# Kernel tuning notes

Measured on AMD Instinct MI355X. Metric: run time of the kernel, lower is better.

Reference implementation:

```python
import jax, jax.numpy as jnp
import numpy as np

B, L, D = 1, 4096, 1024
H = 16
HD = D // H
SCALE = HD ** -0.5


def setup_inputs() -> dict:
    key = jax.random.key(0)
    k1, k2, k3 = jax.random.split(key, 3)
    X = jax.random.normal(k1, (B, L, D), dtype=jnp.float32)
    # torch Linear default init ~ U(-1/sqrt(fan_in), 1/sqrt(fan_in)); scaled normals are fine for a reference
    Wqkv = jax.random.normal(k2, (D, 3 * D), dtype=jnp.float32) * (D ** -0.5)
    bqkv = jnp.zeros((3 * D,), dtype=jnp.float32)
    Wproj = jax.random.normal(k3, (D, D), dtype=jnp.float32) * (D ** -0.5)
    bproj = jnp.zeros((D,), dtype=jnp.float32)
    return {"X": X, "Wqkv": Wqkv, "bqkv": bqkv, "Wproj": Wproj, "bproj": bproj}


def reference(X, Wqkv, bqkv, Wproj, bproj):
    Bn, Ln, Dn = X.shape
    qkv = X @ Wqkv + bqkv                       # [B, L, 3D]
    qkv = qkv.reshape(Bn, Ln, 3, H, HD)
    q, k, v = qkv[:, :, 0], qkv[:, :, 1], qkv[:, :, 2]   # [B, L, H, HD]
    # attention scores [B, H, L, L] (naive, matches original)
    attn = jnp.einsum('bqhd,bkhd->bhqk', q, k) * SCALE
    causal = jnp.tril(jnp.ones((Ln, Ln), dtype=bool))     # True = keep
    attn = jnp.where(causal, attn, -jnp.inf)
    score = jax.nn.softmax(attn, axis=-1)
    out = jnp.einsum('bhqk,bkhd->bqhd', score, v)         # [B, L, H, HD]
    out = out.reshape(Bn, Ln, Dn)
    return out @ Wproj + bproj
```

## Files before the change

### kernel.cpp

```cpp
#include <hip/hip_runtime.h>
#include <hip/hip_bf16.h>
#include <string.h>


typedef unsigned short ushort_t;
typedef __attribute__((ext_vector_type(8))) short short8;
typedef __attribute__((ext_vector_type(4))) float f32x4;

#define MFMA16(a, b, c) __builtin_amdgcn_mfma_f32_16x16x32_bf16(a, b, c, 0, 0, 0)

static constexpr int Lq = 4096;
static constexpr int Dm = 1024;
static constexpr int NH = 16;
static constexpr int HD = 64;
static constexpr int D3 = 3072;
static constexpr float SCALE_LOG2E = 0.125f * 1.44269504088896340736f;

__device__ __forceinline__ ushort_t f2bf(float f) {
    union { float f; unsigned int u; } x{f};
    unsigned int u = x.u;
    u += 0x7fffu + ((u >> 16) & 1u);
    return (ushort_t)(u >> 16);
}

__device__ __forceinline__ unsigned int cvtpk(float a, float b) {
    __hip_bfloat162 h = __float22bfloat162_rn(make_float2(a, b));
    unsigned int u;
    memcpy(&u, &h, 4);
    return u;
}

__device__ __forceinline__ void gl2lds16(const ushort_t* g, ushort_t* l) {
    __builtin_amdgcn_global_load_lds(
        (const __attribute__((address_space(1))) unsigned int*)g,
        (__attribute__((address_space(3))) unsigned int*)l, 16, 0, 0);
}

__global__ void __launch_bounds__(256)
prep(const float* __restrict__ X, const float* __restrict__ Wqkv,
     const float* __restrict__ Wproj, ushort_t* __restrict__ Xb,
     ushort_t* __restrict__ WqkvT, ushort_t* __restrict__ WprojT) {
    __shared__ float tile[32][33];
    const int bid = blockIdx.x, tid = threadIdx.x;
    if (bid < 4096) {
        int i = (bid * 256 + tid) * 4;
        float4 v = *(const float4*)&X[i];
        ushort_t r[4] = { f2bf(v.x), f2bf(v.y), f2bf(v.z), f2bf(v.w) };
        *(uint2*)&Xb[i] = *(uint2*)r;
        return;
    }
    const float* W; ushort_t* Wt; int Nd, nb, kb;
    if (bid < 7168) {
        int b = bid - 4096; W = Wqkv;  Wt = WqkvT;  Nd = 3072;
        nb = (b % 96) * 32; kb = (b / 96) * 32;
    } else {
        int b = bid - 7168; W = Wproj; Wt = WprojT; Nd = 1024;
        nb = (b % 32) * 32; kb = (b / 32) * 32;
    }
    const int tx = tid & 31, ty = tid >> 5;
    for (int j = 0; j < 32; j += 8)
        tile[ty + j][tx] = W[(size_t)(kb + ty + j) * Nd + nb + tx];
    __syncthreads();
    for (int j = 0; j < 32; j += 8)
        Wt[(size_t)(nb + ty + j) * Dm + kb + tx] = f2bf(tile[tx][ty + j]);
}

__global__ void __launch_bounds__(256)
gemm_qkv(const ushort_t* __restrict__ A, const ushort_t* __restrict__ Bt,
         const float* __restrict__ bias, ushort_t* __restrict__ Cq,
         ushort_t* __restrict__ Vt) {
    __shared__ alignas(16) ushort_t Alds[128 * 32];
    __shared__ alignas(16) ushort_t Blds[128 * 32];
    const int tid  = threadIdx.x;
    const int lane = tid & 63;
    const int w    = tid >> 6;
    const int quad = lane >> 4;
    const int l16  = lane & 15;
    const int mbase = blockIdx.x * 128;
    const int nbase = blockIdx.y * 128;
    const int moff  = (w >> 1) * 64;
    const int noff  = (w & 1) * 64;
    const int K = Dm;

    f32x4 acc[4][4] = {};

    for (int kb = 0; kb < K; kb += 32) {
        __syncthreads();
        #pragma unroll
        for (int c = 0; c < 2; c++) {
            int id  = w * 128 + c * 64 + lane;
            int row = id >> 2, col = (id & 3) * 8;
            gl2lds16(&A[(size_t)(mbase + row) * K + kb + col], &Alds[(size_t)(w * 128 + c * 64) * 8]);
            gl2lds16(&Bt[(size_t)(nbase + row) * K + kb + col], &Blds[(size_t)(w * 128 + c * 64) * 8]);
        }
        __syncthreads();
        short8 a[4], b[4];
        #pragma unroll
        for (int m = 0; m < 4; m++)
            a[m] = *(const short8*)&Alds[(moff + m * 16 + l16) * 32 + quad * 8];
        #pragma unroll
        for (int n = 0; n < 4; n++)
            b[n] = *(const short8*)&Blds[(noff + n * 16 + l16) * 32 + quad * 8];
        #pragma unroll
        for (int m = 0; m < 4; m++)
            #pragma unroll
            for (int n = 0; n < 4; n++)
                acc[m][n] = MFMA16(a[m], b[n], acc[m][n]);
    }

    if (nbase < 2048) {
        const bool qscale = (nbase < 1024);
        #pragma unroll
        for (int m = 0; m < 4; m++)
            #pragma unroll
            for (int n = 0; n < 4; n++)
                #pragma unroll
                for (int r = 0; r < 4; r++) {
                    int row = mbase + moff + m * 16 + quad * 4 + r;
                    int col = nbase + noff + n * 16 + l16;
                    float v = acc[m][n][r] + bias[col];
                    if (qscale) v *= SCALE_LOG2E;
                    Cq[(size_t)row * D3 + col] = f2bf(v);
                }
    } else {
        const int dbase = nbase - 2048 + noff;
        const size_t kb0 = (size_t)mbase + moff;
        #pragma unroll
        for (int n = 0; n < 4; n++) {
            const float bv = bias[nbase + noff + n * 16 + l16];
            ushort_t* vrow = Vt + (size_t)(dbase + n * 16 + l16) * Lq + kb0 + quad * 16;
            #pragma unroll
            for (int rp = 0; rp < 2; rp++) {
                ushort_t pk[8];
                #pragma unroll
                for (int dr = 0; dr < 2; dr++)
                    #pragma unroll
                    for (int m = 0; m < 4; m++)
                        pk[dr * 4 + m] = f2bf(acc[m][n][2 * rp + dr] + bv);
                *(short8*)(vrow + rp * 8) = *(const short8*)pk;
            }
        }
    }
}

__global__ void __launch_bounds__(512, 2)
attn_fwd(const ushort_t* __restrict__ qkv, const ushort_t* __restrict__ Vt,
         ushort_t* __restrict__ O) {
    __shared__ alignas(16) ushort_t Kl[2][2][64 * 64];
    __shared__ alignas(16) ushort_t Vl[2][2][64 * 64];
    __shared__ alignas(16) ushort_t Pl[8 * 32 * 72];
    __shared__ alignas(16) float    Ml[256 * 41];

    const int tid  = threadIdx.x;
    const int lane = tid & 63;
    const int w    = tid >> 6;
    const int half = w >> 2;
    const int sub  = w & 3;
    const int quad = lane >> 4;
    const int l16  = lane & 15;
    const int bid  = blockIdx.x;
    const int h    = bid & 15;
    const int p    = bid >> 4;
    ushort_t* pw   = Pl + w * 32 * 72;
    const float NEG_INF = -__builtin_inff();
    const int sw   = l16 & 7;

    const short bf1 = (short)0x3F80;
    const short8 ones = { bf1, bf1, bf1, bf1, bf1, bf1, bf1, bf1 };

    const ushort_t* kbase = qkv + Dm + h * HD;
    const ushort_t* vbase = Vt + (size_t)h * HD * Lq;

    int kvo[4][2];
    #pragma unroll
    for (int s = 0; s < 4; s++)
        #pragma unroll
        for (int kh = 0; kh < 2; kh++)
            kvo[s][kh] = (s * 16 + l16) * 64 + (((kh * 4 + quad) ^ sw) * 8);

    const int rr = tid >> 3, cc = (tid & 7) ^ (rr & 7);
    const ushort_t* kse = kbase + (size_t)rr * D3 + cc * 8;
    const ushort_t* vse = vbase + (size_t)rr * Lq + cc * 8;
    const int dstoff = w * 512;

    for (int sel = 0; sel < 2; sel++) {
        const int c      = sel ? (31 - p) : p;
        const int qc     = c * 128;
        const int rounds = c + 1;
        const int qw     = qc + sub * 32;

        short8 qf[2][2];
        #pragma unroll
        for (int m = 0; m < 2; m++) {
            const ushort_t* qr = qkv + (size_t)(qw + m * 16 + l16) * D3 + h * HD;
            qf[m][0] = *(const short8*)(qr + quad * 8);
            qf[m][1] = *(const short8*)(qr + 32 + quad * 8);
        }

        f32x4 o[2][4] = {};
        f32x4 lacc[2] = {};

        const ushort_t* kp = kse;
        const ushort_t* vp = vse;

        auto stage = [&](int b) {
            gl2lds16(kp,           &Kl[0][b][dstoff]);
            gl2lds16(kp + 64 * D3, &Kl[1][b][dstoff]);
            gl2lds16(vp,           &Vl[0][b][dstoff]);
            gl2lds16(vp + 64,      &Vl[1][b][dstoff]);
            kp += (size_t)128 * D3;
            vp += 128;
        };

        stage(0);

        for (int r = 0; r < rounds; r++) {
            const int buf = r & 1;
            __syncthreads();
            if (r + 1 < rounds) stage(buf ^ 1);

            const ushort_t* Kb = &Kl[half][buf][0];
            const ushort_t* Vb = &Vl[half][buf][0];
            const int k0 = (2 * r + half) * 64;
            const bool domask = (r == rounds - 1);

            short8 kf[4][2];
            #pragma unroll
            for (int s = 0; s < 4; s++)
                #pragma unroll
                for (int kh = 0; kh < 2; kh++)
                    kf[s][kh] = *(const short8*)&Kb[kvo[s][kh]];

            f32x4 st[2][4];
            #pragma unroll
            for (int m = 0; m < 2; m++)
                #pragma unroll
                for (int s = 0; s < 4; s++) {
                    f32x4 t = {};
                    t = MFMA16(qf[m][0], kf[s][0], t);
                    t = MFMA16(qf[m][1], kf[s][1], t);
                    st[m][s] = t;
                }

            #pragma unroll
            for (int m = 0; m < 2; m++)
                #pragma unroll
                for (int r4 = 0; r4 < 4; r4++) {
                    float e[4];
                    #pragma unroll
                    for (int s = 0; s < 4; s++) {
                        float v = st[m][s][r4];
                        if (domask) {
                            const int qg = qw + m * 16 + quad * 4 + r4;
                            if (k0 + s * 16 + l16 > qg) v = NEG_INF;
                        }
                        e[s] = __builtin_amdgcn_exp2f(v);
                    }
                    uint2 pk = { cvtpk(e[0], e[1]), cvtpk(e[2], e[3]) };
                    *(uint2*)&pw[(m * 16 + quad * 4 + r4) * 72 + l16 * 4] = pk;
                }

            short8 pf[2][2];
            #pragma unroll
            for (int m = 0; m < 2; m++)
                #pragma unroll
                for (int kh = 0; kh < 2; kh++)
                    pf[m][kh] = *(const short8*)&pw[(m * 16 + l16) * 72 + kh * 32 + quad * 8];
            #pragma unroll
            for (int m = 0; m < 2; m++) {
                lacc[m] = MFMA16(pf[m][0], ones, lacc[m]);
                lacc[m] = MFMA16(pf[m][1], ones, lacc[m]);
            }

            short8 vf[4][2];
            #pragma unroll
            for (int t = 0; t < 4; t++)
                #pragma unroll
                for (int kh = 0; kh < 2; kh++)
                    vf[t][kh] = *(const short8*)&Vb[kvo[t][kh]];
            #pragma unroll
            for (int m = 0; m < 2; m++)
                #pragma unroll
                for (int t = 0; t < 4; t++) {
                    o[m][t] = MFMA16(pf[m][0], vf[t][0], o[m][t]);
                    o[m][t] = MFMA16(pf[m][1], vf[t][1], o[m][t]);
                }
        }

        __syncthreads();
        if (half == 1) {
            float* dst = Ml + (sub * 64 + lane) * 41;
            #pragma unroll
            for (int m = 0; m < 2; m++)
                #pragma unroll
                for (int t = 0; t < 4; t++)
                    *(f32x4*)(dst + m * 16 + t * 4) = o[m][t];
            *(f32x4*)(dst + 32) = lacc[0];
            *(f32x4*)(dst + 36) = lacc[1];
        }
        __syncthreads();
        if (half == 0) {
            const float* src = Ml + (sub * 64 + lane) * 41;
            #pragma unroll
            for (int m = 0; m < 2; m++)
                #pragma unroll
                for (int t = 0; t < 4; t++)
                    o[m][t] += *(const f32x4*)(src + m * 16 + t * 4);
            lacc[0] += *(const f32x4*)(src + 32);
            lacc[1] += *(const f32x4*)(src + 36);
            #pragma unroll
            for (int m = 0; m < 2; m++)
                #pragma unroll
                for (int r4 = 0; r4 < 4; r4++) {
                    const float inv = 1.0f / lacc[m][r4];
                    ushort_t* orow = O + (size_t)(qw + m * 16 + quad * 4 + r4) * Dm + h * HD;
                    #pragma unroll
                    for (int t = 0; t < 4; t++)
                        orow[t * 16 + l16] = f2bf(o[m][t][r4] * inv);
                }
        }
        __syncthreads();
    }
}

__global__ void __launch_bounds__(256)
gemm_proj(const ushort_t* __restrict__ A, const ushort_t* __restrict__ Bt,
          const float* __restrict__ bias, float* __restrict__ C) {
    __shared__ alignas(16) ushort_t Alds[128 * 32];
    __shared__ alignas(16) ushort_t Blds[64 * 32];
    const int tid  = threadIdx.x;
    const int lane = tid & 63;
    const int w    = tid >> 6;
    const int quad = lane >> 4;
    const int l16  = lane & 15;
    const int mbase = blockIdx.x * 128;
    const int nbase = blockIdx.y * 64;
    const int moff  = (w >> 1) * 64;
    const int noff  = (w & 1) * 32;
    const int K = Dm, N = Dm;

    f32x4 acc[4][2] = {};

    for (int kb = 0; kb < K; kb += 32) {
        __syncthreads();
        #pragma unroll
        for (int c = 0; c < 2; c++) {
            int id  = w * 128 + c * 64 + lane;
            int row = id >> 2, col = (id & 3) * 8;
            gl2lds16(&A[(size_t)(mbase + row) * K + kb + col], &Alds[(size_t)(w * 128 + c * 64) * 8]);
        }
        {
            int id  = w * 64 + lane;
            int row = id >> 2, col = (id & 3) * 8;
            gl2lds16(&Bt[(size_t)(nbase + row) * K + kb + col], &Blds[(size_t)(w * 64) * 8]);
        }
        __syncthreads();
        short8 a[4], b[2];
        #pragma unroll
        for (int m = 0; m < 4; m++)
            a[m] = *(const short8*)&Alds[(moff + m * 16 + l16) * 32 + quad * 8];
        #pragma unroll
        for (int n = 0; n < 2; n++)
            b[n] = *(const short8*)&Blds[(noff + n * 16 + l16) * 32 + quad * 8];
        #pragma unroll
        for (int m = 0; m < 4; m++)
            #pragma unroll
            for (int n = 0; n < 2; n++)
                acc[m][n] = MFMA16(a[m], b[n], acc[m][n]);
    }

    #pragma unroll
    for (int m = 0; m < 4; m++)
        #pragma unroll
        for (int n = 0; n < 2; n++)
            #pragma unroll
            for (int r = 0; r < 4; r++) {
                int row = mbase + moff + m * 16 + quad * 4 + r;
                int col = nbase + noff + n * 16 + l16;
                C[(size_t)row * N + col] = acc[m][n][r] + bias[col];
            }
}

extern "C" void kernel_launch(void* const* d_in, const int* in_sizes, int n_in,
                              void* d_out, int out_size, void* d_ws, size_t ws_size,
                              hipStream_t stream) {
    const float* X     = (const float*)d_in[0];
    const float* Wqkv  = (const float*)d_in[1];
    const float* bqkv  = (const float*)d_in[2];
    const float* Wproj = (const float*)d_in[3];
    const float* bproj = (const float*)d_in[4];
    float* out = (float*)d_out;

    ushort_t* ws     = (ushort_t*)d_ws;
    ushort_t* Xb     = ws;
    ushort_t* WqkvT  = Xb + (size_t)Lq * Dm;
    ushort_t* WprojT = WqkvT + (size_t)D3 * Dm;
    ushort_t* qkvB   = WprojT + (size_t)Dm * Dm;
    ushort_t* VtB    = qkvB + (size_t)Lq * D3;
    ushort_t* Ob     = VtB + (size_t)NH * HD * Lq;

    prep<<<dim3(8192), 256, 0, stream>>>(X, Wqkv, Wproj, Xb, WqkvT, WprojT);

    gemm_qkv<<<dim3(Lq / 128, D3 / 128), 256, 0, stream>>>(
        Xb, WqkvT, bqkv, qkvB, VtB);

    attn_fwd<<<dim3(256), 512, 0, stream>>>(qkvB, VtB, Ob);

    gemm_proj<<<dim3(Lq / 128, Dm / 64), 256, 0, stream>>>(
        Ob, WprojT, bproj, out);
}
```

Measured before the change: 215.2 us.

## Keep P in registers via transposed S=K·Q and 16x16x16 MFMA in attention

Computes scores transposed (K as A operand) so the softmax probabilities come out in a register layout usable directly as the B operand of a 16x16x16 bf16 MFMA for P·V, removing the per-wave P round-trip through LDS and the ones-MFMA row-sum, which is replaced by a register sum plus lane shuffles. The block grows to 1024 threads with four wave groups splitting the KV tile, K and V staging are split across thread halves, and the three-way partial reduction reuses the KV LDS through a union. It risks lower occupancy (one block per CU), halved MFMA K-depth for P·V, and relies on an inline-asm fallback with manual nops when the builtin is missing.

```diff
diff --git a/kernel.cpp b/kernel.cpp
--- a/kernel.cpp
+++ b/kernel.cpp
@@ -5,9 +5,24 @@
 
 typedef unsigned short ushort_t;
 typedef __attribute__((ext_vector_type(8))) short short8;
+typedef __attribute__((ext_vector_type(4))) short short4_t;
 typedef __attribute__((ext_vector_type(4))) float f32x4;
 
 #define MFMA16(a, b, c) __builtin_amdgcn_mfma_f32_16x16x32_bf16(a, b, c, 0, 0, 0)
+
+#if __has_builtin(__builtin_amdgcn_mfma_f32_16x16x16bf16_1k)
+#define HAVE_MFMA16K 1
+__device__ __forceinline__ f32x4 mfma16x16(short4_t a, short4_t b, f32x4 c) {
+    return __builtin_amdgcn_mfma_f32_16x16x16bf16_1k(a, b, c, 0, 0, 0);
+}
+#else
+#define HAVE_MFMA16K 0
+__device__ __forceinline__ f32x4 mfma16x16(short4_t a, short4_t b, f32x4 c) {
+    asm("s_nop 1\n\tv_mfma_f32_16x16x16_bf16 %0, %1, %2, %0"
+        : "+v"(c) : "v"(a), "v"(b));
+    return c;
+}
+#endif
 
 static constexpr int Lq = 4096;
 static constexpr int Dm = 1024;
@@ -143,71 +158,87 @@
     }
 }
 
-__global__ void __launch_bounds__(512, 2)
+__global__ void __launch_bounds__(1024)
 attn_fwd(const ushort_t* __restrict__ qkv, const ushort_t* __restrict__ Vt,
          ushort_t* __restrict__ O) {
-    __shared__ alignas(16) ushort_t Kl[2][2][64 * 64];
-    __shared__ alignas(16) ushort_t Vl[2][2][64 * 64];
-    __shared__ alignas(16) ushort_t Pl[8 * 32 * 72];
-    __shared__ alignas(16) float    Ml[256 * 41];
+    union SMem {
+        struct { ushort_t K[2][2][64 * 64]; ushort_t V[2][2][64 * 64]; } kv;
+        float Ml[3 * 256 * 35];
+    };
+    __shared__ SMem sm;
 
     const int tid  = threadIdx.x;
     const int lane = tid & 63;
     const int w    = tid >> 6;
-    const int half = w >> 2;
+    const int qtr  = w >> 2;
     const int sub  = w & 3;
     const int quad = lane >> 4;
     const int l16  = lane & 15;
     const int bid  = blockIdx.x;
     const int h    = bid & 15;
     const int p    = bid >> 4;
-    ushort_t* pw   = Pl + w * 32 * 72;
     const float NEG_INF = -__builtin_inff();
-    const int sw   = l16 & 7;
-
-    const short bf1 = (short)0x3F80;
-    const short8 ones = { bf1, bf1, bf1, bf1, bf1, bf1, bf1, bf1 };
 
     const ushort_t* kbase = qkv + Dm + h * HD;
     const ushort_t* vbase = Vt + (size_t)h * HD * Lq;
 
-    int kvo[4][2];
+    int koff[2][2];
     #pragma unroll
-    for (int s = 0; s < 4; s++)
+    for (int s = 0; s < 2; s++) {
+        const int tok = (l16 & 3) * 16 + (qtr & 1) * 8 + s * 4 + (l16 >> 2);
+        const int fk  = ((l16 & 3) << 1) | ((l16 >> 2) & 1);
         #pragma unroll
         for (int kh = 0; kh < 2; kh++)
-            kvo[s][kh] = (s * 16 + l16) * 64 + (((kh * 4 + quad) ^ sw) * 8);
-
-    const int rr = tid >> 3, cc = (tid & 7) ^ (rr & 7);
-    const ushort_t* kse = kbase + (size_t)rr * D3 + cc * 8;
-    const ushort_t* vse = vbase + (size_t)rr * Lq + cc * 8;
-    const int dstoff = w * 512;
+            koff[s][kh] = tok * 64 + (((kh * 4 + quad) ^ fk) * 8);
+    }
+    int voff[4][2];
+    #pragma unroll
+    for (int t4 = 0; t4 < 4; t4++)
+        #pragma unroll
+        for (int s = 0; s < 2; s++) {
+            const int row = t4 * 16 + l16;
+            const int g = (qtr & 1) * 4 + s * 2 + (quad >> 1);
+            voff[t4][s] = row * 64 + ((g ^ (l16 & 7)) * 8) + (quad & 1) * 4;
+        }
+    const int kmc = (qtr >> 1) * 64 + (qtr & 1) * 8 + quad;
+
+    const int  tv  = tid & 511;
+    const int  rr  = tv >> 3;
+    const int  ccK = (tv & 7) ^ ((((rr >> 4) & 3) << 1) | (rr & 1));
+    const int  ccV = (tv & 7) ^ (rr & 7);
+    const bool isK = (tid < 512);
+    const int  dsto = (w & 7) * 512;
+    const ushort_t* kse = kbase + (size_t)rr * D3 + ccK * 8;
+    const ushort_t* vse = vbase + (size_t)rr * Lq + ccV * 8;
 
     for (int sel = 0; sel < 2; sel++) {
         const int c      = sel ? (31 - p) : p;
         const int qc     = c * 128;
         const int rounds = c + 1;
-        const int qw     = qc + sub * 32;
+        const int qrow0  = qc + sub * 32;
 
         short8 qf[2][2];
         #pragma unroll
         for (int m = 0; m < 2; m++) {
-            const ushort_t* qr = qkv + (size_t)(qw + m * 16 + l16) * D3 + h * HD;
+            const ushort_t* qr = qkv + (size_t)(qrow0 + m * 16 + l16) * D3 + h * HD;
             qf[m][0] = *(const short8*)(qr + quad * 8);
             qf[m][1] = *(const short8*)(qr + 32 + quad * 8);
         }
 
         f32x4 o[2][4] = {};
-        f32x4 lacc[2] = {};
+        float sacc[2] = { 0.f, 0.f };
 
         const ushort_t* kp = kse;
         const ushort_t* vp = vse;
 
         auto stage = [&](int b) {
-            gl2lds16(kp,           &Kl[0][b][dstoff]);
-            gl2lds16(kp + 64 * D3, &Kl[1][b][dstoff]);
-            gl2lds16(vp,           &Vl[0][b][dstoff]);
-            gl2lds16(vp + 64,      &Vl[1][b][dstoff]);
+            if (isK) {
+                gl2lds16(kp,           &sm.kv.K[0][b][dsto]);
+                gl2lds16(kp + 64 * D3, &sm.kv.K[1][b][dsto]);
+            } else {
+                gl2lds16(vp,           &sm.kv.V[0][b][dsto]);
+                gl2lds16(vp + 64,      &sm.kv.V[1][b][dsto]);
+            }
             kp += (size_t)128 * D3;
             vp += 128;
         };
@@ -219,105 +250,98 @@
             __syncthreads();
             if (r + 1 < rounds) stage(buf ^ 1);
 
-            const ushort_t* Kb = &Kl[half][buf][0];
-            const ushort_t* Vb = &Vl[half][buf][0];
-            const int k0 = (2 * r + half) * 64;
+            const ushort_t* Kb = &sm.kv.K[qtr >> 1][buf][0];
+            const ushort_t* Vb = &sm.kv.V[qtr >> 1][buf][0];
             const bool domask = (r == rounds - 1);
 
-            short8 kf[4][2];
-            #pragma unroll
-            for (int s = 0; s < 4; s++)
+            short8 kf[2][2];
+            #pragma unroll
+            for (int s = 0; s < 2; s++)
                 #pragma unroll
                 for (int kh = 0; kh < 2; kh++)
-                    kf[s][kh] = *(const short8*)&Kb[kvo[s][kh]];
-
-            f32x4 st[2][4];
-            #pragma unroll
-            for (int m = 0; m < 2; m++)
-                #pragma unroll
-                for (int s = 0; s < 4; s++) {
+                    kf[s][kh] = *(const short8*)&Kb[koff[s][kh]];
+
+            short4_t pT[2][2];
+            #pragma unroll
+            for (int m = 0; m < 2; m++) {
+                const int qg = qrow0 + m * 16 + l16;
+                #pragma unroll
+                for (int s = 0; s < 2; s++) {
                     f32x4 t = {};
-                    t = MFMA16(qf[m][0], kf[s][0], t);
-                    t = MFMA16(qf[m][1], kf[s][1], t);
-                    st[m][s] = t;
-                }
-
-            #pragma unroll
-            for (int m = 0; m < 2; m++)
-                #pragma unroll
-                for (int r4 = 0; r4 < 4; r4++) {
+                    t = MFMA16(kf[s][0], qf[m][0], t);
+                    t = MFMA16(kf[s][1], qf[m][1], t);
                     float e[4];
                     #pragma unroll
-                    for (int s = 0; s < 4; s++) {
-                        float v = st[m][s][r4];
-                        if (domask) {
-                            const int qg = qw + m * 16 + quad * 4 + r4;
-                            if (k0 + s * 16 + l16 > qg) v = NEG_INF;
-                        }
-                        e[s] = __builtin_amdgcn_exp2f(v);
+                    for (int r4 = 0; r4 < 4; r4++) {
+                        float v = t[r4];
+                        if (domask && (r * 128 + kmc + s * 4 + r4 * 16 > qg))
+                            v = NEG_INF;
+                        e[r4] = __builtin_amdgcn_exp2f(v);
                     }
-                    uint2 pk = { cvtpk(e[0], e[1]), cvtpk(e[2], e[3]) };
-                    *(uint2*)&pw[(m * 16 + quad * 4 + r4) * 72 + l16 * 4] = pk;
+                    sacc[m] += (e[0] + e[1]) + (e[2] + e[3]);
+                    union { unsigned int u[2]; short4_t s4; } pb;
+                    pb.u[0] = cvtpk(e[0], e[1]);
+                    pb.u[1] = cvtpk(e[2], e[3]);
+                    pT[m][s] = pb.s4;
                 }
-
-            short8 pf[2][2];
+            }
+
+            #pragma unroll
+            for (int t4 = 0; t4 < 4; t4++)
+                #pragma unroll
+                for (int s = 0; s < 2; s++) {
+                    short4_t vf = *(const short4_t*)&Vb[voff[t4][s]];
+                    o[0][t4] = mfma16x16(vf, pT[0][s], o[0][t4]);
+                    o[1][t4] = mfma16x16(vf, pT[1][s], o[1][t4]);
+                }
+        }
+
+#if !HAVE_MFMA16K
+        asm volatile("s_nop 7\n\ts_nop 7" ::: "memory");
+#endif
+        #pragma unroll
+        for (int m = 0; m < 2; m++) {
+            sacc[m] += __shfl_xor(sacc[m], 16);
+            sacc[m] += __shfl_xor(sacc[m], 32);
+        }
+
+        __syncthreads();
+        if (qtr != 0) {
+            float* dst = sm.Ml + (size_t)((qtr - 1) * 256 + sub * 64 + lane) * 35;
             #pragma unroll
             for (int m = 0; m < 2; m++)
                 #pragma unroll
-                for (int kh = 0; kh < 2; kh++)
-                    pf[m][kh] = *(const short8*)&pw[(m * 16 + l16) * 72 + kh * 32 + quad * 8];
+                for (int t4 = 0; t4 < 4; t4++)
+                    *(f32x4*)(dst + (m * 4 + t4) * 4) = o[m][t4];
+            dst[32] = sacc[0];
+            dst[33] = sacc[1];
+        }
+        __syncthreads();
+        if (qtr == 0) {
+            #pragma unroll
+            for (int j = 0; j < 3; j++) {
+                const float* src = sm.Ml + (size_t)(j * 256 + sub * 64 + lane) * 35;
+                #pragma unroll
+                for (int m = 0; m < 2; m++)
+                    #pragma unroll
+                    for (int t4 = 0; t4 < 4; t4++)
+                        o[m][t4] += *(const f32x4*)(src + (m * 4 + t4) * 4);
+                sacc[0] += src[32];
+                sacc[1] += src[33];
+            }
             #pragma unroll
             for (int m = 0; m < 2; m++) {
-                lacc[m] = MFMA16(pf[m][0], ones, lacc[m]);
-                lacc[m] = MFMA16(pf[m][1], ones, lacc[m]);
-            }
-
-            short8 vf[4][2];
-            #pragma unroll
-            for (int t = 0; t < 4; t++)
-                #pragma unroll
-                for (int kh = 0; kh < 2; kh++)
-                    vf[t][kh] = *(const short8*)&Vb[kvo[t][kh]];
-            #pragma unroll
-            for (int m = 0; m < 2; m++)
-                #pragma unroll
-                for (int t = 0; t < 4; t++) {
-                    o[m][t] = MFMA16(pf[m][0], vf[t][0], o[m][t]);
-                    o[m][t] = MFMA16(pf[m][1], vf[t][1], o[m][t]);
+                const float inv = 1.0f / sacc[m];
+                ushort_t* orow = O + (size_t)(qrow0 + m * 16 + l16) * Dm + h * HD;
+                #pragma unroll
+                for (int t4 = 0; t4 < 4; t4++) {
+                    ushort_t pk[4];
+                    #pragma unroll
+                    for (int r4 = 0; r4 < 4; r4++)
+                        pk[r4] = f2bf(o[m][t4][r4] * inv);
+                    *(uint2*)(orow + t4 * 16 + quad * 4) = *(const uint2*)pk;
                 }
-        }
-
-        __syncthreads();
-        if (half == 1) {
-            float* dst = Ml + (sub * 64 + lane) * 41;
-            #pragma unroll
-            for (int m = 0; m < 2; m++)
-                #pragma unroll
-                for (int t = 0; t < 4; t++)
-                    *(f32x4*)(dst + m * 16 + t * 4) = o[m][t];
-            *(f32x4*)(dst + 32) = lacc[0];
-            *(f32x4*)(dst + 36) = lacc[1];
-        }
-        __syncthreads();
-        if (half == 0) {
-            const float* src = Ml + (sub * 64 + lane) * 41;
-            #pragma unroll
-            for (int m = 0; m < 2; m++)
-                #pragma unroll
-                for (int t = 0; t < 4; t++)
-                    o[m][t] += *(const f32x4*)(src + m * 16 + t * 4);
-            lacc[0] += *(const f32x4*)(src + 32);
-            lacc[1] += *(const f32x4*)(src + 36);
-            #pragma unroll
-            for (int m = 0; m < 2; m++)
-                #pragma unroll
-                for (int r4 = 0; r4 < 4; r4++) {
-                    const float inv = 1.0f / lacc[m][r4];
-                    ushort_t* orow = O + (size_t)(qw + m * 16 + quad * 4 + r4) * Dm + h * HD;
-                    #pragma unroll
-                    for (int t = 0; t < 4; t++)
-                        orow[t * 16 + l16] = f2bf(o[m][t][r4] * inv);
-                }
+            }
         }
         __syncthreads();
     }
@@ -404,7 +428,7 @@
     gemm_qkv<<<dim3(Lq / 128, D3 / 128), 256, 0, stream>>>(
         Xb, WqkvT, bqkv, qkvB, VtB);
 
-    attn_fwd<<<dim3(256), 512, 0, stream>>>(qkvB, VtB, Ob);
+    attn_fwd<<<dim3(256), 1024, 0, stream>>>(qkvB, VtB, Ob);
 
     gemm_proj<<<dim3(Lq / 128, Dm / 64), 256, 0, stream>>>(
         Ob, WprojT, bproj, out);
```

After: 211.7 us. About the same (-1.6%).
